# Optimization experiments

Measured on AMD Instinct MI355X. Metric: run time of the kernel, lower is better.

## Reference

```python
import jax, jax.numpy as jnp
import numpy as np

GAMMA = 1.0  # get_gamma(1, None) == 1


def setup_inputs() -> dict:
    key = jax.random.key(0)
    # scale down so recursion divisors 1 - km^2 stay well-conditioned
    a = jax.random.normal(key, (2048, 1024, 33), dtype=jnp.float32) * 0.05
    return {"a": a}


def reference(a):
    # LPC -> PARCOR (reverse Levinson-Durbin recursion), a: [..., M+1]
    M = a.shape[-1] - 1
    K = a[..., :1]          # gain term, passed through
    ar = a[..., 1:] * GAMMA  # working LPC coefficients, length M
    ks = []
    # Python loop over the (small, fixed) LPC order; fully vectorized over batch.
    for m in range(M - 1, -1, -1):
        km = ar[..., m:m + 1]           # reflection coefficient k_m
        ks.append(km)
        if m == 0:
            break
        z = 1.0 - km * km
        k = ar[..., :m]                 # step-down: shrink order by one
        ar = (k - km * k[..., ::-1]) / z
    ks.append(K)
    return jnp.concatenate(ks[::-1], axis=-1)
```

## Files before the change

### kernel.cpp

```cpp
#include <hip/hip_runtime.h>

#define M 32
#define NC 33
#define TPB 128
#define FPB (TPB * NC)
#define V4_ROUNDS 8

__global__ __launch_bounds__(TPB)
void lpc_to_parcor_kernel(const float* __restrict__ a,
                          float* __restrict__ out,
                          long long nrows) {
    __shared__ float lds[FPB];

    const int t = threadIdx.x;
    const long long base = (long long)blockIdx.x * FPB;
    const long long limit = nrows * NC;
    const bool full = (base + FPB) <= limit;

    if (full) {
        const float4* a4 = (const float4*)(a + base);
        float4* lds4 = (float4*)lds;
        #pragma unroll
        for (int k = 0; k < V4_ROUNDS; ++k)
            lds4[t + k * TPB] = a4[t + k * TPB];
        lds[V4_ROUNDS * 4 * TPB + t] = a[base + V4_ROUNDS * 4 * TPB + t];
    } else {
        for (int k = 0; k < NC; ++k) {
            int g = t + k * TPB;
            long long ga = base + g;
            lds[g] = (ga < limit) ? a[ga] : 0.0f;
        }
    }
    __syncthreads();

    const int rb = t * NC;
    float ar[M];
    #pragma unroll
    for (int j = 0; j < M; ++j) ar[j] = lds[rb + 1 + j];

    #pragma unroll
    for (int m = M - 1; m >= 1; --m) {
        float km = ar[m];
        lds[rb + m + 1] = km;
        float z = 1.0f - km * km;
        float r = 1.0f / z;
        const int h = m >> 1;
        #pragma unroll
        for (int j = 0; j < h; ++j) {
            float x = ar[j], y = ar[m - 1 - j];
            ar[j]         = (x - km * y) * r;
            ar[m - 1 - j] = (y - km * x) * r;
        }
        if (m & 1)
            ar[h] = (ar[h] - km * ar[h]) * r;
    }
    lds[rb + 1] = ar[0];
    __syncthreads();

    if (full) {
        float4* o4 = (float4*)(out + base);
        const float4* lds4 = (const float4*)lds;
        #pragma unroll
        for (int k = 0; k < V4_ROUNDS; ++k)
            o4[t + k * TPB] = lds4[t + k * TPB];
        out[base + V4_ROUNDS * 4 * TPB + t] = lds[V4_ROUNDS * 4 * TPB + t];
    } else {
        for (int k = 0; k < NC; ++k) {
            int g = t + k * TPB;
            long long ga = base + g;
            if (ga < limit) out[ga] = lds[g];
        }
    }
}

extern "C" void kernel_launch(void* const* d_in, const int* in_sizes, int n_in,
                              void* d_out, int out_size, void* d_ws, size_t ws_size,
                              hipStream_t stream) {
    const float* a = (const float*)d_in[0];
    float* out = (float*)d_out;
    long long nrows = (long long)in_sizes[0] / NC;
    long long blocks = (nrows + TPB - 1) / TPB;
    lpc_to_parcor_kernel<<<(int)blocks, TPB, 0, stream>>>(a, out, nrows);
}
```

Baseline: 109.4 us.

## Process two tiles per block, prefetching the second into registers during compute

Each block now handles two 128-row tiles. The second tile's global loads are issued into registers before the first tile's recursion runs, so the load latency overlaps with compute. Output stores switch to nontemporal stores. The cost is half as many blocks, which means less parallelism, plus extra register pressure from holding the prefetched vectors, which could lower occupancy.

```diff
diff --git a/kernel.cpp b/kernel.cpp
--- a/kernel.cpp
+++ b/kernel.cpp
@@ -4,72 +4,119 @@
 #define NC 33
 #define TPB 128
 #define FPB (TPB * NC)
-#define V4_ROUNDS 8
+#define V4 8
+#define TAIL (V4 * 4 * TPB)
+
+typedef float f4 __attribute__((ext_vector_type(4)));
+
+__device__ __forceinline__ void levinson(float* __restrict__ lds, int rb) {
+    float ar[M];
+#pragma unroll
+    for (int j = 0; j < M; ++j) ar[j] = lds[rb + 1 + j];
+#pragma unroll
+    for (int m = M - 1; m >= 1; --m) {
+        float km = ar[m];
+        lds[rb + m + 1] = km;
+        float z = 1.0f - km * km;
+        float r = 1.0f / z;
+        const int h = m >> 1;
+#pragma unroll
+        for (int j = 0; j < h; ++j) {
+            float x = ar[j], y = ar[m - 1 - j];
+            ar[j]         = (x - km * y) * r;
+            ar[m - 1 - j] = (y - km * x) * r;
+        }
+        if (m & 1) ar[h] = (ar[h] - km * ar[h]) * r;
+    }
+    lds[rb + 1] = ar[0];
+}
+
+__device__ __forceinline__ void load_tile_full(float* __restrict__ lds,
+                                               const float* __restrict__ src, int t) {
+    const f4* a4 = (const f4*)src;
+    f4* l4 = (f4*)lds;
+#pragma unroll
+    for (int k = 0; k < V4; ++k) l4[t + k * TPB] = a4[t + k * TPB];
+    lds[TAIL + t] = src[TAIL + t];
+}
+
+__device__ __forceinline__ void store_tile_nt(float* __restrict__ dst,
+                                              const float* __restrict__ lds, int t) {
+    const f4* l4 = (const f4*)lds;
+#pragma unroll
+    for (int k = 0; k < V4; ++k) {
+        f4 v = l4[t + k * TPB];
+        __builtin_nontemporal_store(v, (f4*)dst + t + k * TPB);
+    }
+    __builtin_nontemporal_store(lds[TAIL + t], dst + TAIL + t);
+}
+
+__device__ __forceinline__ void process_tile_guarded(float* __restrict__ lds,
+                                                     const float* __restrict__ a,
+                                                     float* __restrict__ out,
+                                                     long long base, long long limit, int t) {
+    for (int k = 0; k < NC; ++k) {
+        int g = t + k * TPB;
+        long long ga = base + g;
+        lds[g] = (ga < limit) ? a[ga] : 0.0f;
+    }
+    __syncthreads();
+    levinson(lds, t * NC);
+    __syncthreads();
+    for (int k = 0; k < NC; ++k) {
+        int g = t + k * TPB;
+        long long ga = base + g;
+        if (ga < limit) out[ga] = lds[g];
+    }
+    __syncthreads();
+}
 
 __global__ __launch_bounds__(TPB)
 void lpc_to_parcor_kernel(const float* __restrict__ a,
                           float* __restrict__ out,
                           long long nrows) {
     __shared__ float lds[FPB];
+    const int t = threadIdx.x;
+    const long long limit = nrows * NC;
+    const long long base0 = (long long)blockIdx.x * 2 * FPB;
+    const long long base1 = base0 + FPB;
+    const bool full0 = (base0 + FPB) <= limit;
+    const bool full1 = (base1 + FPB) <= limit;
 
-    const int t = threadIdx.x;
-    const long long base = (long long)blockIdx.x * FPB;
-    const long long limit = nrows * NC;
-    const bool full = (base + FPB) <= limit;
+    if (full0 && full1) {
+        load_tile_full(lds, a + base0, t);
+        __syncthreads();
 
-    if (full) {
-        const float4* a4 = (const float4*)(a + base);
-        float4* lds4 = (float4*)lds;
-        #pragma unroll
-        for (int k = 0; k < V4_ROUNDS; ++k)
-            lds4[t + k * TPB] = a4[t + k * TPB];
-        lds[V4_ROUNDS * 4 * TPB + t] = a[base + V4_ROUNDS * 4 * TPB + t];
+        f4 p[V4]; float pt;
+        {
+            const f4* b4 = (const f4*)(a + base1);
+#pragma unroll
+            for (int k = 0; k < V4; ++k) p[k] = b4[t + k * TPB];
+            pt = a[base1 + TAIL + t];
+        }
+        __builtin_amdgcn_sched_barrier(0);
+
+        levinson(lds, t * NC);
+        __syncthreads();
+
+        store_tile_nt(out + base0, lds, t);
+        __syncthreads();
+
+        {
+            f4* l4 = (f4*)lds;
+#pragma unroll
+            for (int k = 0; k < V4; ++k) l4[t + k * TPB] = p[k];
+            lds[TAIL + t] = pt;
+        }
+        __syncthreads();
+
+        levinson(lds, t * NC);
+        __syncthreads();
+
+        store_tile_nt(out + base1, lds, t);
     } else {
-        for (int k = 0; k < NC; ++k) {
-            int g = t + k * TPB;
-            long long ga = base + g;
-            lds[g] = (ga < limit) ? a[ga] : 0.0f;
-        }
-    }
-    __syncthreads();
-
-    const int rb = t * NC;
-    float ar[M];
-    #pragma unroll
-    for (int j = 0; j < M; ++j) ar[j] = lds[rb + 1 + j];
-
-    #pragma unroll
-    for (int m = M - 1; m >= 1; --m) {
-        float km = ar[m];
-        lds[rb + m + 1] = km;
-        float z = 1.0f - km * km;
-        float r = 1.0f / z;
-        const int h = m >> 1;
-        #pragma unroll
-        for (int j = 0; j < h; ++j) {
-            float x = ar[j], y = ar[m - 1 - j];
-            ar[j]         = (x - km * y) * r;
-            ar[m - 1 - j] = (y - km * x) * r;
-        }
-        if (m & 1)
-            ar[h] = (ar[h] - km * ar[h]) * r;
-    }
-    lds[rb + 1] = ar[0];
-    __syncthreads();
-
-    if (full) {
-        float4* o4 = (float4*)(out + base);
-        const float4* lds4 = (const float4*)lds;
-        #pragma unroll
-        for (int k = 0; k < V4_ROUNDS; ++k)
-            o4[t + k * TPB] = lds4[t + k * TPB];
-        out[base + V4_ROUNDS * 4 * TPB + t] = lds[V4_ROUNDS * 4 * TPB + t];
-    } else {
-        for (int k = 0; k < NC; ++k) {
-            int g = t + k * TPB;
-            long long ga = base + g;
-            if (ga < limit) out[ga] = lds[g];
-        }
+        if (base0 < limit) process_tile_guarded(lds, a, out, base0, limit, t);
+        if (base1 < limit) process_tile_guarded(lds, a, out, base1, limit, t);
     }
 }
 
@@ -79,6 +126,7 @@
     const float* a = (const float*)d_in[0];
     float* out = (float*)d_out;
     long long nrows = (long long)in_sizes[0] / NC;
-    long long blocks = (nrows + TPB - 1) / TPB;
+    long long tiles = (nrows + TPB - 1) / TPB;
+    long long blocks = (tiles + 1) / 2;
     lpc_to_parcor_kernel<<<(int)blocks, TPB, 0, stream>>>(a, out, nrows);
 }
```

New measurement: 94.80 us. -13.3%, faster.

## Process two rows per thread with packed float2 math and nontemporal stores

Applied to the files above, without the earlier changes.

Each 64-thread block now handles 128 rows, and each thread runs the step-down recursion on two rows at once using float2 vectors. This can map onto packed FP32 instructions and raises instruction-level parallelism. Output stores switch to nontemporal writes to reduce cache pollution. In exchange, register pressure doubles and fewer threads are resident per block, which can lower occupancy for this memory-bound kernel.

```diff
diff --git a/kernel.cpp b/kernel.cpp
--- a/kernel.cpp
+++ b/kernel.cpp
@@ -2,30 +2,34 @@
 
 #define M 32
 #define NC 33
-#define TPB 128
-#define FPB (TPB * NC)
-#define V4_ROUNDS 8
+#define TPB 64
+#define ROWS 128
+#define FPB (ROWS * NC)
+#define V4R 16
+#define TAILF 4096
 
-__global__ __launch_bounds__(TPB)
+typedef float f4 __attribute__((ext_vector_type(4)));
+typedef float f2 __attribute__((ext_vector_type(2)));
+
+__global__ __launch_bounds__(TPB, 2)
 void lpc_to_parcor_kernel(const float* __restrict__ a,
                           float* __restrict__ out,
                           long long nrows) {
     __shared__ float lds[FPB];
-
     const int t = threadIdx.x;
     const long long base = (long long)blockIdx.x * FPB;
     const long long limit = nrows * NC;
     const bool full = (base + FPB) <= limit;
 
     if (full) {
-        const float4* a4 = (const float4*)(a + base);
-        float4* lds4 = (float4*)lds;
-        #pragma unroll
-        for (int k = 0; k < V4_ROUNDS; ++k)
-            lds4[t + k * TPB] = a4[t + k * TPB];
-        lds[V4_ROUNDS * 4 * TPB + t] = a[base + V4_ROUNDS * 4 * TPB + t];
+        const f4* g4 = (const f4*)(a + base);
+        f4* l4 = (f4*)lds;
+#pragma unroll
+        for (int k = 0; k < V4R; ++k)
+            l4[t + k * TPB] = g4[t + k * TPB];
+        ((f2*)(lds + TAILF))[t] = ((const f2*)(a + base + TAILF))[t];
     } else {
-        for (int k = 0; k < NC; ++k) {
+        for (int k = 0; k < 66; ++k) {
             int g = t + k * TPB;
             long long ga = base + g;
             lds[g] = (ga < limit) ? a[ga] : 0.0f;
@@ -33,39 +37,46 @@
     }
     __syncthreads();
 
-    const int rb = t * NC;
-    float ar[M];
-    #pragma unroll
-    for (int j = 0; j < M; ++j) ar[j] = lds[rb + 1 + j];
-
-    #pragma unroll
+    const int rb = t * (2 * NC);
+    f2 ar[M];
+#pragma unroll
+    for (int j = 0; j < M; ++j) {
+        ar[j].x = lds[rb + 1 + j];
+        ar[j].y = lds[rb + NC + 1 + j];
+    }
+#pragma unroll
     for (int m = M - 1; m >= 1; --m) {
-        float km = ar[m];
-        lds[rb + m + 1] = km;
-        float z = 1.0f - km * km;
-        float r = 1.0f / z;
+        f2 km = ar[m];
+        lds[rb + m + 1]      = km.x;
+        lds[rb + NC + m + 1] = km.y;
+        f2 z = 1.0f - km * km;
+        f2 r;
+        r.x = 1.0f / z.x;
+        r.y = 1.0f / z.y;
         const int h = m >> 1;
-        #pragma unroll
+#pragma unroll
         for (int j = 0; j < h; ++j) {
-            float x = ar[j], y = ar[m - 1 - j];
+            f2 x = ar[j], y = ar[m - 1 - j];
             ar[j]         = (x - km * y) * r;
             ar[m - 1 - j] = (y - km * x) * r;
         }
-        if (m & 1)
-            ar[h] = (ar[h] - km * ar[h]) * r;
+        if (m & 1) ar[h] = (ar[h] - km * ar[h]) * r;
     }
-    lds[rb + 1] = ar[0];
+    lds[rb + 1]      = ar[0].x;
+    lds[rb + NC + 1] = ar[0].y;
     __syncthreads();
 
     if (full) {
-        float4* o4 = (float4*)(out + base);
-        const float4* lds4 = (const float4*)lds;
-        #pragma unroll
-        for (int k = 0; k < V4_ROUNDS; ++k)
-            o4[t + k * TPB] = lds4[t + k * TPB];
-        out[base + V4_ROUNDS * 4 * TPB + t] = lds[V4_ROUNDS * 4 * TPB + t];
+        const f4* l4 = (const f4*)lds;
+#pragma unroll
+        for (int k = 0; k < V4R; ++k) {
+            f4 v = l4[t + k * TPB];
+            __builtin_nontemporal_store(v, (f4*)(out + base) + t + k * TPB);
+        }
+        f2 v2 = ((const f2*)(lds + TAILF))[t];
+        __builtin_nontemporal_store(v2, (f2*)(out + base + TAILF) + t);
     } else {
-        for (int k = 0; k < NC; ++k) {
+        for (int k = 0; k < 66; ++k) {
             int g = t + k * TPB;
             long long ga = base + g;
             if (ga < limit) out[ga] = lds[g];
@@ -79,6 +90,6 @@
     const float* a = (const float*)d_in[0];
     float* out = (float*)d_out;
     long long nrows = (long long)in_sizes[0] / NC;
-    long long blocks = (nrows + TPB - 1) / TPB;
-    lpc_to_parcor_kernel<<<(int)blocks, TPB, 0, stream>>>(a, out, nrows);
+    long long ntiles = (nrows + ROWS - 1) / ROWS;
+    lpc_to_parcor_kernel<<<(int)ntiles, TPB, 0, stream>>>(a, out, nrows);
 }
```

After: 93.83 us. 14.2% less time.
